# Performance work log

Hardware: AMD Instinct MI355X
Metric: run time of the kernel (lower is better)

## Reference

```python
import jax, jax.numpy as jnp
from jax import lax
import numpy as np

V, D, H, CO = 50000, 300, 512, 100
B, S, W = 64, 32, 128


def setup_inputs() -> dict:
    key = jax.random.key(0)
    ks = jax.random.split(key, 24)
    sc = 0.1  # mimic uniform(-0.1, 0.1)-style small init; keeps tanh unsaturated
    inp = {
        "paragraphs": jax.random.randint(ks[0], (B, S, W), 0, V, dtype=jnp.int64),
        "embed_table": jax.random.normal(ks[1], (V, D), jnp.float32),
        "conv_w3": jax.random.normal(ks[2], (CO, 1, 3, D), jnp.float32) * 0.05,
        "conv_b3": jax.random.normal(ks[3], (CO,), jnp.float32) * sc,
        "conv_w4": jax.random.normal(ks[4], (CO, 1, 4, D), jnp.float32) * 0.05,
        "conv_b4": jax.random.normal(ks[5], (CO,), jnp.float32) * sc,
        "conv_w5": jax.random.normal(ks[6], (CO, 1, 5, D), jnp.float32) * 0.05,
        "conv_b5": jax.random.normal(ks[7], (CO,), jnp.float32) * sc,
        "proj_w": jax.random.normal(ks[8], (300, 300), jnp.float32) * sc,
        "proj_b": jax.random.normal(ks[9], (300,), jnp.float32) * sc,
        "init_w": jax.random.normal(ks[10], (H, 300), jnp.float32) * sc,
        "init_b": jax.random.normal(ks[11], (H,), jnp.float32) * sc,
        "w_ih_f": jax.random.normal(ks[12], (H, 300), jnp.float32) * sc,
        "w_hh_f": jax.random.normal(ks[13], (H, H), jnp.float32) * sc,
        "b_ih_f": jax.random.normal(ks[14], (H,), jnp.float32) * sc,
        "b_hh_f": jax.random.normal(ks[15], (H,), jnp.float32) * sc,
        "w_ih_b": jax.random.normal(ks[16], (H, 300), jnp.float32) * sc,
        "w_hh_b": jax.random.normal(ks[17], (H, H), jnp.float32) * sc,
        "b_ih_b": jax.random.normal(ks[18], (H,), jnp.float32) * sc,
        "b_hh_b": jax.random.normal(ks[19], (H,), jnp.float32) * sc,
        "cls_w": jax.random.normal(ks[20], (5, 2 * H), jnp.float32) * sc,
        "cls_b": jax.random.normal(ks[21], (5,), jnp.float32) * sc,
    }
    return inp


def _cnn_text(tok, embed_table, conv_params):
    # tok: (N, W) int ids -> (N, 3*CO) sentence features (dropout = eval identity)
    emb = embed_table[tok]              # (N, W, D)
    x = emb[:, None, :, :]              # (N, 1, W, D)
    feats = []
    for w, b in conv_params:
        y = lax.conv_general_dilated(
            x, w, window_strides=(1, 1), padding="VALID",
            dimension_numbers=("NCHW", "OIHW", "NCHW"))  # (N, CO, W-K+1, 1)
        y = jax.nn.relu(y[..., 0] + b[None, :, None])       # (N, CO, W-K+1)
        feats.append(jnp.max(y, axis=2))                    # (N, CO) max-pool over time
    return jnp.concatenate(feats, axis=1)                    # (N, 3*CO)


def reference(paragraphs, embed_table, conv_w3, conv_b3, conv_w4, conv_b4,
              conv_w5, conv_b5, proj_w, proj_b, init_w, init_b,
              w_ih_f, w_hh_f, b_ih_f, b_hh_f, w_ih_b, w_hh_b, b_ih_b, b_hh_b,
              cls_w, cls_b):
    b_, s_, w_ = paragraphs.shape
    tok = paragraphs.reshape(b_ * s_, w_)
    conv_params = [(conv_w3, conv_b3), (conv_w4, conv_b4), (conv_w5, conv_b5)]
    sent = _cnn_text(tok, embed_table, conv_params).reshape(b_, s_, 3 * CO)

    # init_rnn: same init hidden for both directions
    h0 = sent[:, 0, :] @ init_w.T + init_b  # (B, H)

    def step(carry, x_t):
        hf, hb = carry
        xi = x_t @ proj_w.T + proj_b  # (B, 300)
        hf_n = jnp.tanh(xi @ w_ih_f.T + b_ih_f + hf @ w_hh_f.T + b_hh_f)
        hb_n = jnp.tanh(xi @ w_ih_b.T + b_ih_b + hb @ w_hh_b.T + b_hh_b)
        pred = jnp.concatenate([hf_n, hb_n], axis=1) @ cls_w.T + cls_b  # (B, 5)
        return (hf_n, hb_n), pred

    _, preds = lax.scan(step, (h0, h0), jnp.swapaxes(sent, 0, 1))  # (S, B, 5)
    return jnp.swapaxes(preds, 0, 1)  # (B, S, 5)
```

## Files before the change

kernel.cpp:

```cpp
#include <hip/hip_runtime.h>


#define LDSK     304
#define LDSROWB  608
#define LDSBYTES 80384

typedef __bf16   bf16x8 __attribute__((ext_vector_type(8)));
typedef float    f32x16 __attribute__((ext_vector_type(16)));
typedef _Float16 h2v    __attribute__((ext_vector_type(2)));

__global__ void prep_convw(const float* __restrict__ w3, const float* __restrict__ w4,
                           const float* __restrict__ w5, __bf16* __restrict__ Aw32) {
  int idx = blockIdx.x * 256 + threadIdx.x;
  if (idx >= 48 * 20 * 64 * 8) return;
  int i    = idx & 7;
  int lane = (idx >> 3) & 63;
  int rem  = idx >> 9;
  int ks   = rem % 20, g = rem / 20;
  int kc, cg, j; const float* w;
  if (g < 12)      { kc = 3; cg = g / 3;        j = g % 3;        w = w3; }
  else if (g < 28) { kc = 4; cg = (g - 12) / 4; j = (g - 12) % 4; w = w4; }
  else             { kc = 5; cg = (g - 28) / 5; j = (g - 28) % 5; w = w5; }
  int ch = cg * 32 + (lane & 31);
  int k  = ks * 16 + (lane >> 5) * 8 + i;
  float v = 0.f;
  if (ch < 100 && k < 300) v = w[(ch * kc + j) * 300 + k];
  Aw32[idx] = (__bf16)v;
}

__device__ __forceinline__ unsigned int packf16(float a, float b) {
  h2v h; h[0] = (_Float16)a; h[1] = (_Float16)b;
  return __builtin_bit_cast(unsigned int, h);
}
__global__ void prep_whh(const float* __restrict__ whf, const float* __restrict__ whb,
                         uint4* __restrict__ Wq) {
  int idx = blockIdx.x * 256 + threadIdx.x;
  if (idx >= 2 * 128 * 256) return;
  int dir = idx >> 15;
  int rem = idx & 32767;
  int kq = rem >> 8, tid = rem & 255;
  const float* W = dir ? whb : whf;
  const float* r0 = W + (size_t)tid * 512 + 4 * kq;
  const float* r1 = W + (size_t)(tid + 256) * 512 + 4 * kq;
  uint4 o;
  o.x = packf16(r0[0], r0[1]);
  o.y = packf16(r1[0], r1[1]);
  o.z = packf16(r0[2], r0[3]);
  o.w = packf16(r1[2], r1[3]);
  Wq[idx] = o;
}

__device__ __forceinline__ void conv_chunk32(const char* ldsc, const __bf16* __restrict__ Aw32,
                                             int GB, int kc, int cg0,
                                             const float* __restrict__ bias,
                                             int colbase, int pmax,
                                             float* __restrict__ srow, int lane) {
  const int m32 = lane & 31, hi = lane >> 5;
  f32x16 acc[2][4];
#pragma unroll
  for (int i = 0; i < 2; ++i)
#pragma unroll
    for (int n = 0; n < 4; ++n)
#pragma unroll
      for (int e = 0; e < 16; ++e) acc[i][n][e] = 0.f;

  for (int j = 0; j < kc; ++j) {
    const int row0 = m32 + j;
    const int mask = (row0 & 7) << 4;
    const int rowbyte = row0 * LDSROWB + hi * 16;
    const __bf16* a0 = Aw32 + ((size_t)((GB + cg0 * kc + j) * 20) << 9) + lane * 8;
    const __bf16* a1 = Aw32 + ((size_t)((GB + (cg0 + 1) * kc + j) * 20) << 9) + lane * 8;
#pragma unroll 2
    for (int ks = 0; ks < 20; ++ks) {
      bf16x8 bf[4];
#pragma unroll
      for (int nt = 0; nt < 4; ++nt) {
        int addr = rowbyte + nt * (32 * LDSROWB) + ks * 32;
        bf[nt] = *(const bf16x8*)(ldsc + (addr ^ mask));
      }
      bf16x8 af0 = *(const bf16x8*)(a0 + (ks << 9));
      bf16x8 af1 = *(const bf16x8*)(a1 + (ks << 9));
#pragma unroll
      for (int nt = 0; nt < 4; ++nt)
        acc[0][nt] = __builtin_amdgcn_mfma_f32_32x32x16_bf16(af0, bf[nt], acc[0][nt], 0, 0, 0);
#pragma unroll
      for (int nt = 0; nt < 4; ++nt)
        acc[1][nt] = __builtin_amdgcn_mfma_f32_32x32x16_bf16(af1, bf[nt], acc[1][nt], 0, 0, 0);
    }
  }
#pragma unroll
  for (int i = 0; i < 2; ++i) {
    float m[16];
#pragma unroll
    for (int r = 0; r < 16; ++r) m[r] = -3.0e38f;
#pragma unroll
    for (int nt = 0; nt < 4; ++nt) {
      int p = nt * 32 + m32;
      bool valid = (p <= pmax);
#pragma unroll
      for (int r = 0; r < 16; ++r)
        m[r] = fmaxf(m[r], valid ? acc[i][nt][r] : -3.0e38f);
    }
#pragma unroll
    for (int r = 0; r < 16; ++r) {
#pragma unroll
      for (int d = 1; d < 32; d <<= 1) m[r] = fmaxf(m[r], __shfl_xor(m[r], d, 64));
    }
    if (m32 == 0) {
#pragma unroll
      for (int r = 0; r < 16; ++r) {
        int ch = (cg0 + i) * 32 + (r & 3) + 8 * (r >> 2) + 4 * hi;
        if (ch < 100) srow[colbase + ch] = fmaxf(m[r] + bias[ch], 0.f);
      }
    }
  }
}

__global__ void __launch_bounds__(256, 2)
conv_kernel(const int* __restrict__ tok, const float* __restrict__ emb,
            const __bf16* __restrict__ Aw32,
            const float* __restrict__ b3, const float* __restrict__ b4, const float* __restrict__ b5,
            float* __restrict__ sent) {
  extern __shared__ __bf16 lds[];
  char* ldsc = (char*)lds;
  const int sid = blockIdx.x, tid = threadIdx.x;
  for (int i = tid; i < LDSBYTES / 4; i += 256) ((unsigned int*)lds)[i] = 0u;
  __syncthreads();
  const int* t0 = tok + sid * 128;
  for (int i = tid; i < 128 * 75; i += 256) {
    int r = i / 75, q = i - r * 75;
    long tk = (long)t0[r];
    float4 v = *(const float4*)(emb + tk * 300L + q * 4);
    union { __bf16 h[4]; uint2 u; } pk;
    pk.h[0] = (__bf16)v.x; pk.h[1] = (__bf16)v.y; pk.h[2] = (__bf16)v.z; pk.h[3] = (__bf16)v.w;
    int wb = (r * LDSROWB + q * 8) ^ ((r & 7) << 4);
    *(uint2*)(ldsc + wb) = pk.u;
  }
  __syncthreads();
  const int wave = tid >> 6, lane = tid & 63;
  float* srow = sent + (size_t)sid * 304;
  switch (wave) {
    case 0:
      conv_chunk32(ldsc, Aw32, 28, 5, 0, b5, 200, 123, srow, lane);
      break;
    case 1:
      conv_chunk32(ldsc, Aw32, 28, 5, 2, b5, 200, 123, srow, lane);
      break;
    case 2:
      conv_chunk32(ldsc, Aw32, 12, 4, 0, b4, 100, 124, srow, lane);
      conv_chunk32(ldsc, Aw32,  0, 3, 0, b3,   0, 125, srow, lane);
      break;
    default:
      conv_chunk32(ldsc, Aw32, 12, 4, 2, b4, 100, 124, srow, lane);
      conv_chunk32(ldsc, Aw32,  0, 3, 2, b3,   0, 125, srow, lane);
      break;
  }
}

__global__ void xigh0_kernel(const float* __restrict__ sent,
                             const float* __restrict__ pw, const float* __restrict__ pb,
                             const float* __restrict__ wf, const float* __restrict__ wb,
                             const float* __restrict__ bif, const float* __restrict__ bhf,
                             const float* __restrict__ bib, const float* __restrict__ bhb,
                             const float* __restrict__ iw, const float* __restrict__ ib,
                             float* __restrict__ G, float* __restrict__ h0) {
  __shared__ float s[8][300];
  __shared__ float xi[8][304];
  const int tid = threadIdx.x;
  if (blockIdx.x < 256) {
    const int rb = blockIdx.x * 8;
    for (int i = tid; i < 8 * 300; i += 256) {
      int r = i / 300, c = i - r * 300;
      s[r][c] = sent[(size_t)(rb + r) * 304 + c];
    }
    __syncthreads();
    for (int o = tid; o < 300; o += 256) {
      const float* w = pw + o * 300;
      float bvv = pb[o];
      float a[8];
#pragma unroll
      for (int r = 0; r < 8; ++r) a[r] = bvv;
      for (int k = 0; k < 300; k += 4) {
        float4 wv = *(const float4*)(w + k);
#pragma unroll
        for (int r = 0; r < 8; ++r)
          a[r] += wv.x * s[r][k] + wv.y * s[r][k + 1] + wv.z * s[r][k + 2] + wv.w * s[r][k + 3];
      }
#pragma unroll
      for (int r = 0; r < 8; ++r) xi[r][o] = a[r];
    }
    __syncthreads();
    for (int o = tid; o < 1024; o += 256) {
      int dir = o >> 9, oo = o & 511;
      const float* w = (dir ? wb : wf) + oo * 300;
      float bvv = dir ? (bib[oo] + bhb[oo]) : (bif[oo] + bhf[oo]);
      float a[8];
#pragma unroll
      for (int r = 0; r < 8; ++r) a[r] = bvv;
      for (int k = 0; k < 300; k += 4) {
        float4 wv = *(const float4*)(w + k);
#pragma unroll
        for (int r = 0; r < 8; ++r)
          a[r] += wv.x * xi[r][k] + wv.y * xi[r][k + 1] + wv.z * xi[r][k + 2] + wv.w * xi[r][k + 3];
      }
#pragma unroll
      for (int r = 0; r < 8; ++r) G[(rb + r) * 1024 + o] = a[r];
    }
  } else {
    const int bb = (blockIdx.x - 256) * 8;
    for (int i = tid; i < 8 * 300; i += 256) {
      int r = i / 300, c = i - r * 300;
      s[r][c] = sent[(size_t)((bb + r) * 32) * 304 + c];
    }
    __syncthreads();
    for (int o = tid; o < 512; o += 256) {
      const float* w = iw + o * 300;
      float bvv = ib[o];
      float a[8];
#pragma unroll
      for (int r = 0; r < 8; ++r) a[r] = bvv;
      for (int k = 0; k < 300; k += 4) {
        float4 wv = *(const float4*)(w + k);
#pragma unroll
        for (int r = 0; r < 8; ++r)
          a[r] += wv.x * s[r][k] + wv.y * s[r][k + 1] + wv.z * s[r][k + 2] + wv.w * s[r][k + 3];
      }
#pragma unroll
      for (int r = 0; r < 8; ++r) h0[(bb + r) * 512 + o] = a[r];
    }
  }
}

#if __has_builtin(__builtin_amdgcn_fdot2)
#define FDOT2(a, b, c) __builtin_amdgcn_fdot2((a), (b), (c), false)
#else
static __device__ __forceinline__ float FDOT2(h2v a, h2v b, float c) {
  return c + (float)a[0] * (float)b[0] + (float)a[1] * (float)b[1];
}
#endif
__device__ __forceinline__ h2v as_h2(unsigned int u) { return __builtin_bit_cast(h2v, u); }

__global__ void __launch_bounds__(256)
rnn_kernel(const uint4* __restrict__ Wq, const float* __restrict__ G,
           const float* __restrict__ h0, float* __restrict__ H) {
  const int blk = blockIdx.x, tid = threadIdx.x;
  const int dir = blk >> 6, b = blk & 63;
  __shared__ float hs[512];
  __shared__ uint2 h2p[128];
  for (int i = tid; i < 512; i += 256) hs[i] = h0[b * 512 + i];
  __syncthreads();
  const uint4* W = Wq + (size_t)dir * (128 * 256);
  for (int t = 0; t < 32; ++t) {
    { h2v hh; hh[0] = (_Float16)hs[2 * tid]; hh[1] = (_Float16)hs[2 * tid + 1];
      ((unsigned int*)h2p)[tid] = __builtin_bit_cast(unsigned int, hh); }
    __syncthreads();
    const float* g = G + ((size_t)(b * 32 + t)) * 1024 + dir * 512;
    float s0[4], s1[4];
    s0[0] = g[tid]; s1[0] = g[tid + 256];
    s0[1] = s0[2] = s0[3] = 0.f;
    s1[1] = s1[2] = s1[3] = 0.f;
#pragma unroll 2
    for (int kb = 0; kb < 32; ++kb) {
#pragma unroll
      for (int u = 0; u < 4; ++u) {
        int kq = kb * 4 + u;
        uint4 wv = W[kq * 256 + tid];
        uint2 hp = h2p[kq];
        h2v p = as_h2(hp.x), q = as_h2(hp.y);
        s0[u] = FDOT2(as_h2(wv.x), p, s0[u]);
        s1[u] = FDOT2(as_h2(wv.y), p, s1[u]);
        s0[u] = FDOT2(as_h2(wv.z), q, s0[u]);
        s1[u] = FDOT2(as_h2(wv.w), q, s1[u]);
      }
    }
    float a0 = (s0[0] + s0[1]) + (s0[2] + s0[3]);
    float a1 = (s1[0] + s1[1]) + (s1[2] + s1[3]);
    __syncthreads();
    float n0 = tanhf(a0), n1 = tanhf(a1);
    hs[tid] = n0; hs[tid + 256] = n1;
    float* Ht = H + ((size_t)((dir * 64 + b) * 32 + t)) * 512;
    Ht[tid] = n0; Ht[tid + 256] = n1;
    __syncthreads();
  }
}

__global__ void pred_kernel(const float* __restrict__ H, const float* __restrict__ cw,
                            const float* __restrict__ cb, float* __restrict__ out) {
  const int bt = blockIdx.x;
  const int lane = threadIdx.x;
  const int b = bt >> 5, t = bt & 31;
  const float* hf = H + ((size_t)(b * 32 + t)) * 512;
  const float* hb = H + ((size_t)((64 + b) * 32 + t)) * 512;
  for (int c = 0; c < 5; ++c) {
    const float* w = cw + c * 1024;
    float a = 0.f;
    for (int o = lane; o < 512; o += 64) a += w[o] * hf[o] + w[512 + o] * hb[o];
#pragma unroll
    for (int d = 32; d; d >>= 1) a += __shfl_down(a, d, 64);
    if (lane == 0) out[bt * 5 + c] = a + cb[c];
  }
}

extern "C" void kernel_launch(void* const* d_in, const int* in_sizes, int n_in,
                              void* d_out, int out_size, void* d_ws, size_t ws_size,
                              hipStream_t stream) {
  const int*   tok  = (const int*)d_in[0];
  const float* emb  = (const float*)d_in[1];
  const float* w3   = (const float*)d_in[2];
  const float* b3   = (const float*)d_in[3];
  const float* w4   = (const float*)d_in[4];
  const float* b4   = (const float*)d_in[5];
  const float* w5   = (const float*)d_in[6];
  const float* b5   = (const float*)d_in[7];
  const float* pw   = (const float*)d_in[8];
  const float* pb   = (const float*)d_in[9];
  const float* iw   = (const float*)d_in[10];
  const float* ib   = (const float*)d_in[11];
  const float* wihf = (const float*)d_in[12];
  const float* whhf = (const float*)d_in[13];
  const float* bihf = (const float*)d_in[14];
  const float* bhhf = (const float*)d_in[15];
  const float* wihb = (const float*)d_in[16];
  const float* whhb = (const float*)d_in[17];
  const float* bihb = (const float*)d_in[18];
  const float* bhhb = (const float*)d_in[19];
  const float* cw   = (const float*)d_in[20];
  const float* cb   = (const float*)d_in[21];
  float* out = (float*)d_out;

  char* ws = (char*)d_ws;
  __bf16* Aw32  = (__bf16*)(ws);
  uint4* Wq     = (uint4*)(ws +  1u * 1024 * 1024);
  float* sent   = (float*)(ws +  2u * 1024 * 1024);
  float* G      = (float*)(ws +  8u * 1024 * 1024);
  float* h0     = (float*)(ws + 16u * 1024 * 1024);
  float* H      = (float*)(ws + 17u * 1024 * 1024);

  prep_convw<<<1920, 256, 0, stream>>>(w3, w4, w5, Aw32);
  prep_whh<<<256, 256, 0, stream>>>(whhf, whhb, Wq);

  hipFuncSetAttribute(reinterpret_cast<const void*>(conv_kernel),
                      hipFuncAttributeMaxDynamicSharedMemorySize, LDSBYTES);
  conv_kernel<<<2048, 256, LDSBYTES, stream>>>(tok, emb, Aw32, b3, b4, b5, sent);

  xigh0_kernel<<<264, 256, 0, stream>>>(sent, pw, pb, wihf, wihb, bihf, bhhf, bihb, bhhb,
                                        iw, ib, G, h0);
  rnn_kernel<<<128, 256, 0, stream>>>(Wq, G, h0, H);
  pred_kernel<<<2048, 64, 0, stream>>>(H, cw, cb, out);
}
```

Baseline: 642.3 us.

## Pre-convert embedding table to bf16, trim conv K loop, split RNN reduction

Adds a pass that converts the entire 50000x300 embedding table to bf16 before the conv kernel, so the gather reads half the bytes and skips per-element conversion. The conv K loop drops from 20 to 19 steps of 16 (304 covers 300), and only the padding regions of LDS are zeroed instead of the whole buffer. The RNN kernel moves to 512 threads, splitting the k reduction across two halves and combining them through shared memory to shorten the serial dot product per step. The full-table conversion touches 60MB every call, which may cost more than the gather of about 262K rows it saves, and the bf16 table shares workspace with G, which is only written later.

```diff
diff --git a/kernel.cpp b/kernel.cpp
--- a/kernel.cpp
+++ b/kernel.cpp
@@ -3,20 +3,33 @@
 
 #define LDSK     304
 #define LDSROWB  608
-#define LDSBYTES 80384
+#define LDSBYTES 80256
 
 typedef __bf16   bf16x8 __attribute__((ext_vector_type(8)));
 typedef float    f32x16 __attribute__((ext_vector_type(16)));
 typedef _Float16 h2v    __attribute__((ext_vector_type(2)));
 
+#define MFMA32(a, b, c) __builtin_amdgcn_mfma_f32_32x32x16_bf16((a), (b), (c), 0, 0, 0)
+
+__global__ void prep_emb(const float* __restrict__ e, __bf16* __restrict__ eh) {
+  long i = ((long)blockIdx.x * 256 + threadIdx.x) * 8;
+  if (i >= 15000000L) return;
+  float4 a = *(const float4*)(e + i);
+  float4 b = *(const float4*)(e + i + 4);
+  union { __bf16 h[8]; uint4 u; } pk;
+  pk.h[0] = (__bf16)a.x; pk.h[1] = (__bf16)a.y; pk.h[2] = (__bf16)a.z; pk.h[3] = (__bf16)a.w;
+  pk.h[4] = (__bf16)b.x; pk.h[5] = (__bf16)b.y; pk.h[6] = (__bf16)b.z; pk.h[7] = (__bf16)b.w;
+  *(uint4*)(eh + i) = pk.u;
+}
+
 __global__ void prep_convw(const float* __restrict__ w3, const float* __restrict__ w4,
                            const float* __restrict__ w5, __bf16* __restrict__ Aw32) {
   int idx = blockIdx.x * 256 + threadIdx.x;
-  if (idx >= 48 * 20 * 64 * 8) return;
+  if (idx >= 48 * 19 * 64 * 8) return;
   int i    = idx & 7;
   int lane = (idx >> 3) & 63;
   int rem  = idx >> 9;
-  int ks   = rem % 20, g = rem / 20;
+  int ks   = rem % 19, g = rem / 19;
   int kc, cg, j; const float* w;
   if (g < 12)      { kc = 3; cg = g / 3;        j = g % 3;        w = w3; }
   else if (g < 28) { kc = 4; cg = (g - 12) / 4; j = (g - 12) % 4; w = w4; }
@@ -68,24 +81,24 @@
     const int row0 = m32 + j;
     const int mask = (row0 & 7) << 4;
     const int rowbyte = row0 * LDSROWB + hi * 16;
-    const __bf16* a0 = Aw32 + ((size_t)((GB + cg0 * kc + j) * 20) << 9) + lane * 8;
-    const __bf16* a1 = Aw32 + ((size_t)((GB + (cg0 + 1) * kc + j) * 20) << 9) + lane * 8;
+    const __bf16* a0 = Aw32 + (size_t)(GB + cg0 * kc + j) * (19 * 512) + lane * 8;
+    const __bf16* a1 = Aw32 + (size_t)(GB + (cg0 + 1) * kc + j) * (19 * 512) + lane * 8;
 #pragma unroll 2
-    for (int ks = 0; ks < 20; ++ks) {
+    for (int ks = 0; ks < 19; ++ks) {
       bf16x8 bf[4];
 #pragma unroll
       for (int nt = 0; nt < 4; ++nt) {
         int addr = rowbyte + nt * (32 * LDSROWB) + ks * 32;
         bf[nt] = *(const bf16x8*)(ldsc + (addr ^ mask));
       }
-      bf16x8 af0 = *(const bf16x8*)(a0 + (ks << 9));
-      bf16x8 af1 = *(const bf16x8*)(a1 + (ks << 9));
+      bf16x8 af0 = *(const bf16x8*)(a0 + ks * 512);
+      bf16x8 af1 = *(const bf16x8*)(a1 + ks * 512);
 #pragma unroll
       for (int nt = 0; nt < 4; ++nt)
-        acc[0][nt] = __builtin_amdgcn_mfma_f32_32x32x16_bf16(af0, bf[nt], acc[0][nt], 0, 0, 0);
+        acc[0][nt] = MFMA32(af0, bf[nt], acc[0][nt]);
 #pragma unroll
       for (int nt = 0; nt < 4; ++nt)
-        acc[1][nt] = __builtin_amdgcn_mfma_f32_32x32x16_bf16(af1, bf[nt], acc[1][nt], 0, 0, 0);
+        acc[1][nt] = MFMA32(af1, bf[nt], acc[1][nt]);
     }
   }
 #pragma unroll
@@ -117,24 +130,27 @@
 }
 
 __global__ void __launch_bounds__(256, 2)
-conv_kernel(const int* __restrict__ tok, const float* __restrict__ emb,
+conv_kernel(const int* __restrict__ tok, const __bf16* __restrict__ embh,
             const __bf16* __restrict__ Aw32,
             const float* __restrict__ b3, const float* __restrict__ b4, const float* __restrict__ b5,
             float* __restrict__ sent) {
   extern __shared__ __bf16 lds[];
   char* ldsc = (char*)lds;
   const int sid = blockIdx.x, tid = threadIdx.x;
-  for (int i = tid; i < LDSBYTES / 4; i += 256) ((unsigned int*)lds)[i] = 0u;
-  __syncthreads();
   const int* t0 = tok + sid * 128;
+  const char* eb = (const char*)embh;
+  for (int i = tid; i < 4 * 76; i += 256) {
+    int r = 128 + i / 76, q = i - (i / 76) * 76;
+    *(uint2*)(ldsc + ((r * LDSROWB + q * 8) ^ ((r & 7) << 4))) = (uint2){0u, 0u};
+  }
+  if (tid < 128) {
+    *(uint2*)(ldsc + ((tid * LDSROWB + 600) ^ ((tid & 7) << 4))) = (uint2){0u, 0u};
+  }
   for (int i = tid; i < 128 * 75; i += 256) {
     int r = i / 75, q = i - r * 75;
     long tk = (long)t0[r];
-    float4 v = *(const float4*)(emb + tk * 300L + q * 4);
-    union { __bf16 h[4]; uint2 u; } pk;
-    pk.h[0] = (__bf16)v.x; pk.h[1] = (__bf16)v.y; pk.h[2] = (__bf16)v.z; pk.h[3] = (__bf16)v.w;
-    int wb = (r * LDSROWB + q * 8) ^ ((r & 7) << 4);
-    *(uint2*)(ldsc + wb) = pk.u;
+    uint2 v = *(const uint2*)(eb + tk * 600L + q * 8);
+    *(uint2*)(ldsc + ((r * LDSROWB + q * 8) ^ ((r & 7) << 4))) = v;
   }
   __syncthreads();
   const int wave = tid >> 6, lane = tid & 63;
@@ -240,46 +256,44 @@
 #endif
 __device__ __forceinline__ h2v as_h2(unsigned int u) { return __builtin_bit_cast(h2v, u); }
 
-__global__ void __launch_bounds__(256)
+__global__ void __launch_bounds__(512)
 rnn_kernel(const uint4* __restrict__ Wq, const float* __restrict__ G,
            const float* __restrict__ h0, float* __restrict__ H) {
   const int blk = blockIdx.x, tid = threadIdx.x;
   const int dir = blk >> 6, b = blk & 63;
+  const int o = tid & 255, kh = tid >> 8;
   __shared__ float hs[512];
   __shared__ uint2 h2p[128];
-  for (int i = tid; i < 512; i += 256) hs[i] = h0[b * 512 + i];
+  __shared__ float part[2][512];
+  if (tid < 512) { hs[tid] = h0[b * 512 + tid]; }
   __syncthreads();
   const uint4* W = Wq + (size_t)dir * (128 * 256);
   for (int t = 0; t < 32; ++t) {
-    { h2v hh; hh[0] = (_Float16)hs[2 * tid]; hh[1] = (_Float16)hs[2 * tid + 1];
-      ((unsigned int*)h2p)[tid] = __builtin_bit_cast(unsigned int, hh); }
-    __syncthreads();
-    const float* g = G + ((size_t)(b * 32 + t)) * 1024 + dir * 512;
-    float s0[4], s1[4];
-    s0[0] = g[tid]; s1[0] = g[tid + 256];
-    s0[1] = s0[2] = s0[3] = 0.f;
-    s1[1] = s1[2] = s1[3] = 0.f;
-#pragma unroll 2
-    for (int kb = 0; kb < 32; ++kb) {
-#pragma unroll
-      for (int u = 0; u < 4; ++u) {
-        int kq = kb * 4 + u;
-        uint4 wv = W[kq * 256 + tid];
-        uint2 hp = h2p[kq];
-        h2v p = as_h2(hp.x), q = as_h2(hp.y);
-        s0[u] = FDOT2(as_h2(wv.x), p, s0[u]);
-        s1[u] = FDOT2(as_h2(wv.y), p, s1[u]);
-        s0[u] = FDOT2(as_h2(wv.z), q, s0[u]);
-        s1[u] = FDOT2(as_h2(wv.w), q, s1[u]);
-      }
-    }
-    float a0 = (s0[0] + s0[1]) + (s0[2] + s0[3]);
-    float a1 = (s1[0] + s1[1]) + (s1[2] + s1[3]);
-    __syncthreads();
-    float n0 = tanhf(a0), n1 = tanhf(a1);
-    hs[tid] = n0; hs[tid + 256] = n1;
-    float* Ht = H + ((size_t)((dir * 64 + b) * 32 + t)) * 512;
-    Ht[tid] = n0; Ht[tid + 256] = n1;
+    if (tid < 256) ((unsigned int*)h2p)[tid] = packf16(hs[2 * tid], hs[2 * tid + 1]);
+    __syncthreads();
+    float a0 = 0.f, a1 = 0.f, c0 = 0.f, c1 = 0.f;
+    const int kbase = kh * 64;
+#pragma unroll 4
+    for (int kk = 0; kk < 64; kk += 2) {
+      int k0 = kbase + kk, k1 = k0 + 1;
+      uint4 w0 = W[k0 * 256 + o]; uint2 p0 = h2p[k0];
+      uint4 w1 = W[k1 * 256 + o]; uint2 p1 = h2p[k1];
+      a0 = FDOT2(as_h2(w0.x), as_h2(p0.x), a0); a0 = FDOT2(as_h2(w0.z), as_h2(p0.y), a0);
+      a1 = FDOT2(as_h2(w0.y), as_h2(p0.x), a1); a1 = FDOT2(as_h2(w0.w), as_h2(p0.y), a1);
+      c0 = FDOT2(as_h2(w1.x), as_h2(p1.x), c0); c0 = FDOT2(as_h2(w1.z), as_h2(p1.y), c0);
+      c1 = FDOT2(as_h2(w1.y), as_h2(p1.x), c1); c1 = FDOT2(as_h2(w1.w), as_h2(p1.y), c1);
+    }
+    part[kh][o] = a0 + c0;
+    part[kh][o + 256] = a1 + c1;
+    __syncthreads();
+    if (kh == 0) {
+      const float* g = G + (size_t)(b * 32 + t) * 1024 + dir * 512;
+      float n0 = tanhf(g[o]       + part[0][o]       + part[1][o]);
+      float n1 = tanhf(g[o + 256] + part[0][o + 256] + part[1][o + 256]);
+      hs[o] = n0; hs[o + 256] = n1;
+      float* Ht = H + (size_t)((dir * 64 + b) * 32 + t) * 512;
+      Ht[o] = n0; Ht[o + 256] = n1;
+    }
     __syncthreads();
   }
 }
@@ -332,19 +346,21 @@
   __bf16* Aw32  = (__bf16*)(ws);
   uint4* Wq     = (uint4*)(ws +  1u * 1024 * 1024);
   float* sent   = (float*)(ws +  2u * 1024 * 1024);
+  __bf16* embh  = (__bf16*)(ws + 8u * 1024 * 1024);
   float* G      = (float*)(ws +  8u * 1024 * 1024);
   float* h0     = (float*)(ws + 16u * 1024 * 1024);
   float* H      = (float*)(ws + 17u * 1024 * 1024);
 
-  prep_convw<<<1920, 256, 0, stream>>>(w3, w4, w5, Aw32);
+  prep_emb<<<7325, 256, 0, stream>>>(emb, embh);
+  prep_convw<<<1824, 256, 0, stream>>>(w3, w4, w5, Aw32);
   prep_whh<<<256, 256, 0, stream>>>(whhf, whhb, Wq);
 
   hipFuncSetAttribute(reinterpret_cast<const void*>(conv_kernel),
                       hipFuncAttributeMaxDynamicSharedMemorySize, LDSBYTES);
-  conv_kernel<<<2048, 256, LDSBYTES, stream>>>(tok, emb, Aw32, b3, b4, b5, sent);
+  conv_kernel<<<2048, 256, LDSBYTES, stream>>>(tok, embh, Aw32, b3, b4, b5, sent);
 
   xigh0_kernel<<<264, 256, 0, stream>>>(sent, pw, pb, wihf, wihb, bihf, bhhf, bihb, bhhb,
                                         iw, ib, G, h0);
-  rnn_kernel<<<128, 256, 0, stream>>>(Wq, G, h0, H);
+  rnn_kernel<<<128, 512, 0, stream>>>(Wq, G, h0, H);
   pred_kernel<<<2048, 64, 0, stream>>>(H, cw, cb, out);
 }
```

Result: faster. 602.9 us (-6.1%).
